# Optimization experiments

Hardware: AMD Instinct MI355X
Metric: run time of the kernel (lower is better)

Reference implementation:

```python
import jax, jax.numpy as jnp
import numpy as np

B, C, S, HEADS, MLP = 8, 128, 32, 8, 512
EPS = 1e-5
SCALE = (C // HEADS) ** -0.5  # dim_head=16 -> 16**-0.5


def setup_inputs() -> dict:
    key = jax.random.key(0)
    ks = jax.random.split(key, 6)
    x = jax.random.normal(ks[0], (B, C, S, S, S), jnp.float32)
    qkv_w = jax.random.normal(ks[1], (3 * C, C), jnp.float32) * 0.02   # Conv3d 1x1x1, no bias
    proj_w = jax.random.normal(ks[2], (C, C), jnp.float32) * 0.02
    proj_b = jnp.zeros((C,), jnp.float32)
    ln1_w = jnp.ones((C, S, S, S), jnp.float32)
    ln1_b = jnp.zeros((C, S, S, S), jnp.float32)
    ln2_w = jnp.ones((C, S, S, S), jnp.float32)
    ln2_b = jnp.zeros((C, S, S, S), jnp.float32)
    mlp_w1 = jax.random.normal(ks[3], (MLP, C), jnp.float32) * 0.02
    mlp_b1 = jnp.zeros((MLP,), jnp.float32)
    mlp_w2 = jax.random.normal(ks[4], (C, MLP), jnp.float32) * 0.02
    mlp_b2 = jnp.zeros((C,), jnp.float32)
    return dict(x=x, qkv_w=qkv_w, proj_w=proj_w, proj_b=proj_b,
                ln1_w=ln1_w, ln1_b=ln1_b, ln2_w=ln2_w, ln2_b=ln2_b,
                mlp_w1=mlp_w1, mlp_b1=mlp_b1, mlp_w2=mlp_w2, mlp_b2=mlp_b2)


def _layernorm_full(x, w, b):
    # LayerNorm over (channel, D, H, W) per batch element, biased variance, eps=1e-5
    mu = jnp.mean(x, axis=(1, 2, 3, 4), keepdims=True)
    var = jnp.mean(jnp.square(x - mu), axis=(1, 2, 3, 4), keepdims=True)
    return (x - mu) * jax.lax.rsqrt(var + EPS) * w[None] + b[None]


def _block(x, qkv_w, proj_w, proj_b, ln1_w, ln1_b, ln2_w, ln2_b,
           mlp_w1, mlp_b1, mlp_w2, mlp_b2):
    b, c, d, h, w = x.shape
    n = d * h * w
    ch = c // HEADS
    xf = x.reshape(b, c, n)
    # 1x1x1 conv == per-voxel matmul over channels
    qkv = jnp.einsum('bcn,oc->bon', xf, qkv_w)                 # [b, 3c, n]
    q, k, v = jnp.split(qkv, 3, axis=1)
    q = q.reshape(b, HEADS, ch, n)
    k = k.reshape(b, HEADS, ch, n)
    v = v.reshape(b, HEADS, ch, n)
    # channel-channel attention: contraction over spatial tokens n
    attn = jax.nn.softmax(jnp.einsum('bhin,bhjn->bhij', q, k) * SCALE, axis=-1)
    out = jnp.einsum('bhij,bhjn->bhin', attn, v).reshape(b, c, n)
    out = jnp.einsum('bcn,oc->bon', out, proj_w) + proj_b[None, :, None]
    x1 = _layernorm_full(x + out.reshape(b, c, d, h, w), ln1_w, ln1_b)
    # MLP: conv1x1 -> exact GELU -> conv1x1
    x1f = x1.reshape(b, c, n)
    hid = jax.nn.gelu(jnp.einsum('bcn,oc->bon', x1f, mlp_w1) + mlp_b1[None, :, None],
                      approximate=False)
    m = jnp.einsum('bon,co->bcn', hid, mlp_w2) + mlp_b2[None, :, None]
    return _layernorm_full(x1 + m.reshape(b, c, d, h, w), ln2_w, ln2_b)


def reference(x, qkv_w, proj_w, proj_b, ln1_w, ln1_b, ln2_w, ln2_b,
              mlp_w1, mlp_b1, mlp_w2, mlp_b2):
    return _block(x, qkv_w, proj_w, proj_b, ln1_w, ln1_b, ln2_w, ln2_b,
                  mlp_w1, mlp_b1, mlp_w2, mlp_b2)
```

## Files before the change

kernel.cpp:

```cpp
#include <hip/hip_runtime.h>
#include <hip/hip_bf16.h>
#include <math.h>


#define N_SP 32768
typedef __hip_bfloat16 bf16;
static const size_t DS = (size_t)128 * N_SP;

typedef __attribute__((ext_vector_type(8))) short s8b;
typedef __attribute__((ext_vector_type(4))) float f4;

__device__ __forceinline__ ushort f2b(float f) {
    __hip_bfloat16 h = __float2bfloat16(f);
    return *reinterpret_cast<ushort*>(&h);
}
__device__ __forceinline__ float b2f(ushort u) {
    unsigned v = ((unsigned)u) << 16;
    float f;
    __builtin_memcpy(&f, &v, 4);
    return f;
}
__device__ __forceinline__ float gelu_f(float h) {
    float u = 1.5957691216057308f * h * fmaf(0.044715f, h * h, 1.0f);
    float e = __expf(u);
    return h * (1.0f - __builtin_amdgcn_rcpf(e + 1.0f));
}
__device__ __forceinline__ int swz8(int n, int c0) {
    return n * 128 + (c0 ^ ((n & 15) << 3));
}
__device__ __forceinline__ int swz4(int n, int c0) {
    return n * 128 + (((c0 & 0x78) ^ ((n & 15) << 3)) | (c0 & 4));
}

__global__ __launch_bounds__(256) void k_transpose(const float* __restrict__ in,
                                                   float* __restrict__ out,
                                                   int R, int Ccols) {
    int idx = blockIdx.x * 256 + threadIdx.x;
    if (idx >= R * Ccols) return;
    int r = idx / Ccols, c = idx % Ccols;
    out[c * R + r] = in[idx];
}

__global__ __launch_bounds__(256) void k_cvt(const float* __restrict__ in,
                                             ushort* __restrict__ out, int n) {
    int i = blockIdx.x * 256 + threadIdx.x;
    if (i < n) out[i] = f2b(in[i]);
}

__global__ __launch_bounds__(256) void k_packln(const float* __restrict__ w,
                                                const float* __restrict__ b,
                                                uint* __restrict__ out) {
    int tid = blockIdx.x * 256 + threadIdx.x;
    int c = tid >> 15, n = tid & 32767;
    uint lo = f2b(w[tid]);
    uint hi = f2b(b[tid]);
    out[(size_t)n * 128 + c] = lo | (hi << 16);
}

__global__ __launch_bounds__(256) void k_packflat(const float* __restrict__ w,
                                                  const float* __restrict__ b,
                                                  uint* __restrict__ out) {
    int tid = blockIdx.x * 256 + threadIdx.x;
    uint lo = f2b(w[tid]);
    uint hi = f2b(b[tid]);
    out[tid] = lo | (hi << 16);
}

__global__ __launch_bounds__(256, 4) void k_cov(const float* __restrict__ x,
                                                float* __restrict__ Gpart) {
    __shared__ ushort xs[128 * 136];
    const int kb = blockIdx.x, b = blockIdx.y;
    const int t = threadIdx.x;
    const int wave = t >> 6, lane = t & 63, q = lane >> 4, r = lane & 15;
    f4 acc[8][2];
#pragma unroll
    for (int m = 0; m < 8; ++m) { acc[m][0] = (f4){0,0,0,0}; acc[m][1] = (f4){0,0,0,0}; }
    for (int ch = 0; ch < 2; ++ch) {
        const int nbase = kb * 256 + ch * 128;
        __syncthreads();
        {
            const int nq = t & 31, cr = t >> 5;
            const float* xp = x + (size_t)b * DS + nbase + nq * 4;
#pragma unroll
            for (int half = 0; half < 2; ++half) {
                float4 xv[8];
#pragma unroll
                for (int cc = 0; cc < 8; ++cc)
                    xv[cc] = *(const float4*)(xp + (size_t)(cr * 16 + half * 8 + cc) * N_SP);
#pragma unroll
                for (int cc = 0; cc < 8; ++cc) {
                    int c = cr * 16 + half * 8 + cc;
                    ushort4 pk;
                    pk.x = f2b(xv[cc].x); pk.y = f2b(xv[cc].y);
                    pk.z = f2b(xv[cc].z); pk.w = f2b(xv[cc].w);
                    *(ushort4*)&xs[c * 136 + nq * 4] = pk;
                }
            }
        }
        __syncthreads();
        for (int kk = 0; kk < 4; ++kk) {
            const int c0 = kk * 32 + q * 8;
            s8b bj0 = *(const s8b*)&xs[(wave * 32 + r) * 136 + c0];
            s8b bj1 = *(const s8b*)&xs[(wave * 32 + 16 + r) * 136 + c0];
#pragma unroll
            for (int m = 0; m < 8; ++m) {
                s8b a = *(const s8b*)&xs[(m * 16 + r) * 136 + c0];
                acc[m][0] = __builtin_amdgcn_mfma_f32_16x16x32_bf16(a, bj0, acc[m][0], 0, 0, 0);
                acc[m][1] = __builtin_amdgcn_mfma_f32_16x16x32_bf16(a, bj1, acc[m][1], 0, 0, 0);
            }
        }
    }
    float* gp = Gpart + ((size_t)b * 128 + kb) * 16384;
#pragma unroll
    for (int n2 = 0; n2 < 2; ++n2)
#pragma unroll
        for (int m = 0; m < 8; ++m)
#pragma unroll
            for (int rg = 0; rg < 4; ++rg) {
                int i = m * 16 + q * 4 + rg;
                int j = wave * 32 + n2 * 16 + r;
                gp[i * 128 + j] = acc[m][n2][rg];
            }
}

__global__ __launch_bounds__(256) void k_greduce(const float* __restrict__ Gpart,
                                                 float* __restrict__ G) {
    int tid = blockIdx.x * 256 + threadIdx.x;
    int b = tid >> 14, ij = tid & 16383;
    float s = 0.f;
#pragma unroll 8
    for (int kb = 0; kb < 128; ++kb)
        s += Gpart[((size_t)b * 128 + kb) * 16384 + ij];
    G[tid] = s;
}

__global__ __launch_bounds__(256) void k_gram_small(const float* __restrict__ G,
                                                    const float* __restrict__ qkv_w,
                                                    float* __restrict__ attn) {
    __shared__ float t1[16 * 132];
    __shared__ float sg[16 * 16];
    const int bh = blockIdx.x;
    const int b = bh >> 3, h = bh & 7;
    const int t = threadIdx.x;
    {
        const int i = t >> 4, c20 = (t & 15) * 8;
        const float* wq = qkv_w + (size_t)(h * 16 + i) * 128;
        const float* Gb = G + (size_t)b * 16384;
        float a[8];
#pragma unroll
        for (int k = 0; k < 8; ++k) a[k] = 0.f;
        for (int c = 0; c < 128; ++c) {
            float w = wq[c];
            const float* grow = Gb + c * 128 + c20;
#pragma unroll
            for (int k = 0; k < 8; ++k) a[k] = fmaf(w, grow[k], a[k]);
        }
#pragma unroll
        for (int k = 0; k < 8; ++k) t1[i * 132 + c20 + k] = a[k];
    }
    __syncthreads();
    {
        const int i = t >> 4, j = t & 15;
        const float* wk = qkv_w + (size_t)(128 + h * 16 + j) * 128;
        float s = 0.f;
        for (int c2 = 0; c2 < 128; ++c2) s = fmaf(t1[i * 132 + c2], wk[c2], s);
        sg[i * 16 + j] = s * 0.25f;
    }
    __syncthreads();
    if (t < 16) {
        float mx = -1e30f;
#pragma unroll
        for (int j = 0; j < 16; ++j) mx = fmaxf(mx, sg[t * 16 + j]);
        float e[16], sum = 0.f;
#pragma unroll
        for (int j = 0; j < 16; ++j) { e[j] = expf(sg[t * 16 + j] - mx); sum += e[j]; }
        float inv = 1.0f / sum;
#pragma unroll
        for (int j = 0; j < 16; ++j)
            attn[((size_t)bh * 16 + t) * 16 + j] = e[j] * inv;
    }
}

__global__ __launch_bounds__(256, 2) void k_mfold(const float* __restrict__ attn,
                                                  const float* __restrict__ qkv_w,
                                                  const float* __restrict__ PT,
                                                  ushort* __restrict__ Mbb) {
    __shared__ float t2[128 * 128];
    const int b = blockIdx.x, t = threadIdx.x;
    {
        const int hi = t >> 1, c0 = (t & 1) * 64;
        const int h = hi >> 4;
        const float* at = attn + ((size_t)b * 128 + hi) * 16;
        float a[16];
#pragma unroll
        for (int j = 0; j < 16; ++j) a[j] = at[j];
        float sc[64];
#pragma unroll
        for (int c = 0; c < 64; ++c) sc[c] = 0.f;
        for (int j = 0; j < 16; ++j) {
            const float* wv = qkv_w + (size_t)(256 + h * 16 + j) * 128 + c0;
            float aj = a[j];
#pragma unroll
            for (int c = 0; c < 64; ++c) sc[c] = fmaf(aj, wv[c], sc[c]);
        }
#pragma unroll
        for (int c = 0; c < 64; ++c) t2[hi * 128 + c0 + c] = sc[c];
    }
    __syncthreads();
    const int c = t & 127, half = t >> 7;
    float acc[128];
#pragma unroll
    for (int o = 0; o < 128; ++o) acc[o] = 0.f;
    for (int ci = half * 64; ci < half * 64 + 64; ++ci) {
        float s = t2[ci * 128 + c];
        const float* pt = PT + ci * 128;
#pragma unroll
        for (int o = 0; o < 128; ++o) acc[o] = fmaf(pt[o], s, acc[o]);
    }
    __syncthreads();
    if (half) {
#pragma unroll
        for (int o = 0; o < 128; ++o) t2[c * 128 + o] = acc[o];
    }
    __syncthreads();
    if (!half) {
        ushort* m = Mbb + (size_t)b * 16384;
#pragma unroll
        for (int o = 0; o < 128; ++o)
            m[(size_t)o * 128 + c] = f2b(acc[o] + t2[c * 128 + o]);
    }
}

__global__ __launch_bounds__(256, 3) void k_attnproj(const float* __restrict__ x,
                                                     const ushort* __restrict__ Mbb,
                                                     const float* __restrict__ proj_b,
                                                     ushort* __restrict__ x1Tb,
                                                     float* __restrict__ st) {
    __shared__ ushort xT[128 * 136];
    const int b = blockIdx.y;
    const int n0 = blockIdx.x * 128;
    const int t = threadIdx.x;
    const int wave = t >> 6, lane = t & 63, q = lane >> 4, r = lane & 15;
    {
        const int nn = t & 127, cg = t >> 7;
        const float* xp = x + (size_t)b * DS + n0 + nn;
        for (int gb = 0; gb < 4; ++gb) {
            float xv[16];
#pragma unroll
            for (int u = 0; u < 16; ++u)
                xv[u] = xp[(size_t)(cg * 64 + gb * 16 + u) * N_SP];
#pragma unroll
            for (int u4 = 0; u4 < 4; ++u4) {
                int c0 = cg * 64 + gb * 16 + u4 * 4;
                ushort4 pk;
                pk.x = f2b(xv[u4 * 4 + 0]); pk.y = f2b(xv[u4 * 4 + 1]);
                pk.z = f2b(xv[u4 * 4 + 2]); pk.w = f2b(xv[u4 * 4 + 3]);
                *(ushort4*)&xT[nn * 136 + c0] = pk;
            }
        }
    }
    const int orow = wave * 32 + r;
    s8b a[8];
    {
        const ushort* mp = Mbb + (size_t)b * 16384 + (size_t)orow * 128 + q * 8;
#pragma unroll
        for (int m = 0; m < 2; ++m)
#pragma unroll
            for (int kk = 0; kk < 4; ++kk)
                a[m * 4 + kk] = *(const s8b*)(mp + m * 16 * 128 + kk * 32);
    }
    __syncthreads();
    f4 acc[2][8];
#pragma unroll
    for (int m = 0; m < 2; ++m)
#pragma unroll
        for (int j = 0; j < 8; ++j) acc[m][j] = (f4){0,0,0,0};
#pragma unroll
    for (int kk = 0; kk < 4; ++kk) {
        const int c0 = kk * 32 + q * 8;
#pragma unroll
        for (int j = 0; j < 8; ++j) {
            s8b bx = *(const s8b*)&xT[(j * 16 + r) * 136 + c0];
            acc[0][j] = __builtin_amdgcn_mfma_f32_16x16x32_bf16(a[kk],     bx, acc[0][j], 0, 0, 0);
            acc[1][j] = __builtin_amdgcn_mfma_f32_16x16x32_bf16(a[4 + kk], bx, acc[1][j], 0, 0, 0);
        }
    }
    float s = 0.f, sq = 0.f;
    float4 pbq0 = *(const float4*)&proj_b[wave * 32 + q * 4];
    float4 pbq1 = *(const float4*)&proj_b[wave * 32 + 16 + q * 4];
#pragma unroll
    for (int m = 0; m < 2; ++m) {
        const int o0 = wave * 32 + m * 16 + q * 4;
        const float4 pb = m ? pbq1 : pbq0;
#pragma unroll
        for (int j = 0; j < 8; ++j) {
            const int nn = j * 16 + r;
            ushort4 xr = *(const ushort4*)&xT[nn * 136 + o0];
            float v0 = acc[m][j][0] + pb.x + b2f(xr.x);
            float v1 = acc[m][j][1] + pb.y + b2f(xr.y);
            float v2 = acc[m][j][2] + pb.z + b2f(xr.z);
            float v3 = acc[m][j][3] + pb.w + b2f(xr.w);
            ushort4 ov;
            ov.x = f2b(v0); ov.y = f2b(v1); ov.z = f2b(v2); ov.w = f2b(v3);
            *(ushort4*)(x1Tb + (size_t)b * DS + (size_t)(n0 + nn) * 128 + o0) = ov;
            s += (v0 + v1) + (v2 + v3);
            sq = fmaf(v0, v0, sq); sq = fmaf(v1, v1, sq);
            sq = fmaf(v2, v2, sq); sq = fmaf(v3, v3, sq);
        }
    }
#pragma unroll
    for (int off = 32; off > 0; off >>= 1) {
        s += __shfl_down(s, off, 64);
        sq += __shfl_down(sq, off, 64);
    }
    if (lane == 0) {
        atomicAdd(&st[0 + b], s);
        atomicAdd(&st[8 + b], sq);
    }
}

__global__ void k_finalize(float* st, int off) {
    int b = threadIdx.x;
    if (b < 8) {
        const float invn = 1.0f / 4194304.0f;
        float mu = st[off + b] * invn;
        float var = st[off + 8 + b] * invn - mu * mu;
        st[off + 16 + b] = mu;
        st[off + 24 + b] = rsqrtf(var + 1e-5f);
    }
}

__global__ __launch_bounds__(256) void k_lnapply(const float* __restrict__ in,
                                                 const uint* __restrict__ lnwb,
                                                 const float* __restrict__ st, int off,
                                                 float* __restrict__ out) {
    size_t i4 = (size_t)blockIdx.x * 256 + threadIdx.x;
    int b = (int)(i4 >> 20);
    size_t cn = i4 * 4 - (size_t)b * 4194304;
    float mu = st[off + 16 + b], rs = st[off + 24 + b];
    const float4 xv = *(const float4*)(in + (size_t)b * DS + cn);
    const uint4 wv = *(const uint4*)(lnwb + cn);
    float4 o;
    o.x = fmaf((xv.x - mu) * rs, b2f((ushort)(wv.x & 0xffffu)), b2f((ushort)(wv.x >> 16)));
    o.y = fmaf((xv.y - mu) * rs, b2f((ushort)(wv.y & 0xffffu)), b2f((ushort)(wv.y >> 16)));
    o.z = fmaf((xv.z - mu) * rs, b2f((ushort)(wv.z & 0xffffu)), b2f((ushort)(wv.z >> 16)));
    o.w = fmaf((xv.w - mu) * rs, b2f((ushort)(wv.w & 0xffffu)), b2f((ushort)(wv.w >> 16)));
    *(float4*)(out + (size_t)b * DS + cn) = o;
}

__global__ __launch_bounds__(256, 2) void k_mlp(const ushort* __restrict__ x1Tb,
                                                float* __restrict__ xout,
                                                const ushort* __restrict__ w1b,
                                                const float* __restrict__ b1v,
                                                const ushort* __restrict__ w2b,
                                                const float* __restrict__ b2v,
                                                const uint* __restrict__ lnwbT,
                                                float* __restrict__ st) {
    __shared__ ushort xT[128 * 128];
    __shared__ ushort hT[128 * 128];
    const int b = blockIdx.y;
    const int n0 = blockIdx.x * 128;
    const int t = threadIdx.x;
    const int wave = t >> 6, lane = t & 63, q = lane >> 4, r = lane & 15;
    const float mu = st[16 + b], rs = st[24 + b];
    {
        const int c8 = (t & 15) * 8, rb = t >> 4;
        const ushort* xb = x1Tb + (size_t)b * DS + (size_t)n0 * 128;
        const uint*  wb = lnwbT + (size_t)n0 * 128;
#pragma unroll
        for (int gb = 0; gb < 2; ++gb) {
            s8b xv[4]; uint4 wv0[4], wv1[4];
#pragma unroll
            for (int u = 0; u < 4; ++u) {
                int nn = (gb * 4 + u) * 16 + rb;
                xv[u]  = *(const s8b*)(xb + (size_t)nn * 128 + c8);
                wv0[u] = *(const uint4*)(wb + (size_t)nn * 128 + c8);
                wv1[u] = *(const uint4*)(wb + (size_t)nn * 128 + c8 + 4);
            }
#pragma unroll
            for (int u = 0; u < 4; ++u) {
                int nn = (gb * 4 + u) * 16 + rb;
                ushort4 p0, p1;
                float xe;
                xe = b2f((ushort)xv[u][0]);
                p0.x = f2b(fmaf((xe - mu) * rs, b2f((ushort)(wv0[u].x & 0xffffu)), b2f((ushort)(wv0[u].x >> 16))));
                xe = b2f((ushort)xv[u][1]);
                p0.y = f2b(fmaf((xe - mu) * rs, b2f((ushort)(wv0[u].y & 0xffffu)), b2f((ushort)(wv0[u].y >> 16))));
                xe = b2f((ushort)xv[u][2]);
                p0.z = f2b(fmaf((xe - mu) * rs, b2f((ushort)(wv0[u].z & 0xffffu)), b2f((ushort)(wv0[u].z >> 16))));
                xe = b2f((ushort)xv[u][3]);
                p0.w = f2b(fmaf((xe - mu) * rs, b2f((ushort)(wv0[u].w & 0xffffu)), b2f((ushort)(wv0[u].w >> 16))));
                xe = b2f((ushort)xv[u][4]);
                p1.x = f2b(fmaf((xe - mu) * rs, b2f((ushort)(wv1[u].x & 0xffffu)), b2f((ushort)(wv1[u].x >> 16))));
                xe = b2f((ushort)xv[u][5]);
                p1.y = f2b(fmaf((xe - mu) * rs, b2f((ushort)(wv1[u].y & 0xffffu)), b2f((ushort)(wv1[u].y >> 16))));
                xe = b2f((ushort)xv[u][6]);
                p1.z = f2b(fmaf((xe - mu) * rs, b2f((ushort)(wv1[u].z & 0xffffu)), b2f((ushort)(wv1[u].z >> 16))));
                xe = b2f((ushort)xv[u][7]);
                p1.w = f2b(fmaf((xe - mu) * rs, b2f((ushort)(wv1[u].w & 0xffffu)), b2f((ushort)(wv1[u].w >> 16))));
                *(ushort4*)&xT[swz4(nn, c8)] = p0;
                *(ushort4*)&xT[swz4(nn, c8 + 4)] = p1;
            }
        }
    }
    const int orow = wave * 32 + r;
    s8b a1[8];
    {
        const ushort* w1p = w1b + (size_t)orow * 128 + q * 8;
#pragma unroll
        for (int m = 0; m < 2; ++m)
#pragma unroll
            for (int kk = 0; kk < 4; ++kk)
                a1[m * 4 + kk] = *(const s8b*)(w1p + m * 16 * 128 + kk * 32);
    }
    __syncthreads();
    f4 acc2[2][8];
#pragma unroll
    for (int m = 0; m < 2; ++m)
#pragma unroll
        for (int j = 0; j < 8; ++j) acc2[m][j] = (f4){0,0,0,0};

    for (int os = 0; os < 4; ++os) {
        f4 acc1[2][8];
#pragma unroll
        for (int m = 0; m < 2; ++m)
#pragma unroll
            for (int j = 0; j < 8; ++j) acc1[m][j] = (f4){0,0,0,0};
#pragma unroll
        for (int kk = 0; kk < 4; ++kk) {
            const int c0 = kk * 32 + q * 8;
#pragma unroll
            for (int j = 0; j < 8; ++j) {
                s8b bx = *(const s8b*)&xT[swz8(j * 16 + r, c0)];
                acc1[0][j] = __builtin_amdgcn_mfma_f32_16x16x32_bf16(a1[kk],     bx, acc1[0][j], 0, 0, 0);
                acc1[1][j] = __builtin_amdgcn_mfma_f32_16x16x32_bf16(a1[4 + kk], bx, acc1[1][j], 0, 0, 0);
            }
        }
        s8b a2[8];
        {
            const ushort* w2p = w2b + (size_t)orow * 512 + os * 128 + q * 8;
#pragma unroll
            for (int m = 0; m < 2; ++m)
#pragma unroll
                for (int kk = 0; kk < 4; ++kk)
                    a2[m * 4 + kk] = *(const s8b*)(w2p + m * 16 * 512 + kk * 32);
        }
        float4 b1q0 = *(const float4*)&b1v[os * 128 + wave * 32 + q * 4];
        float4 b1q1 = *(const float4*)&b1v[os * 128 + wave * 32 + 16 + q * 4];
#pragma unroll
        for (int m = 0; m < 2; ++m) {
            const int hr0 = wave * 32 + m * 16 + q * 4;
            const float4 bq = m ? b1q1 : b1q0;
#pragma unroll
            for (int j = 0; j < 8; ++j) {
                ushort4 pk;
                pk.x = f2b(gelu_f(acc1[m][j][0] + bq.x));
                pk.y = f2b(gelu_f(acc1[m][j][1] + bq.y));
                pk.z = f2b(gelu_f(acc1[m][j][2] + bq.z));
                pk.w = f2b(gelu_f(acc1[m][j][3] + bq.w));
                *(ushort4*)&hT[swz4(j * 16 + r, hr0)] = pk;
            }
        }
        __syncthreads();
#pragma unroll
        for (int kk = 0; kk < 4; ++kk) {
            const int c0 = kk * 32 + q * 8;
#pragma unroll
            for (int j = 0; j < 8; ++j) {
                s8b hx = *(const s8b*)&hT[swz8(j * 16 + r, c0)];
                acc2[0][j] = __builtin_amdgcn_mfma_f32_16x16x32_bf16(a2[kk],     hx, acc2[0][j], 0, 0, 0);
                acc2[1][j] = __builtin_amdgcn_mfma_f32_16x16x32_bf16(a2[4 + kk], hx, acc2[1][j], 0, 0, 0);
            }
        }
        if (os < 3) {
            const ushort* w1p = w1b + (size_t)((os + 1) * 128 + orow) * 128 + q * 8;
#pragma unroll
            for (int m = 0; m < 2; ++m)
#pragma unroll
                for (int kk = 0; kk < 4; ++kk)
                    a1[m * 4 + kk] = *(const s8b*)(w1p + m * 16 * 128 + kk * 32);
        }
        __syncthreads();
    }
    float s = 0.f, sq = 0.f;
    float4 b2q0 = *(const float4*)&b2v[wave * 32 + q * 4];
    float4 b2q1 = *(const float4*)&b2v[wave * 32 + 16 + q * 4];
#pragma unroll
    for (int m = 0; m < 2; ++m) {
        const int o0 = wave * 32 + m * 16 + q * 4;
        const float4 bq = m ? b2q1 : b2q0;
#pragma unroll
        for (int j = 0; j < 8; ++j) {
            const int nn = j * 16 + r;
            ushort4 xr = *(const ushort4*)&xT[swz4(nn, o0)];
            float v0 = acc2[m][j][0] + bq.x + b2f(xr.x);
            float v1 = acc2[m][j][1] + bq.y + b2f(xr.y);
            float v2 = acc2[m][j][2] + bq.z + b2f(xr.z);
            float v3 = acc2[m][j][3] + bq.w + b2f(xr.w);
            float* op = xout + (size_t)b * DS + n0 + nn;
            op[(size_t)(o0 + 0) * N_SP] = v0;
            op[(size_t)(o0 + 1) * N_SP] = v1;
            op[(size_t)(o0 + 2) * N_SP] = v2;
            op[(size_t)(o0 + 3) * N_SP] = v3;
            s += (v0 + v1) + (v2 + v3);
            sq = fmaf(v0, v0, sq); sq = fmaf(v1, v1, sq);
            sq = fmaf(v2, v2, sq); sq = fmaf(v3, v3, sq);
        }
    }
#pragma unroll
    for (int off = 32; off > 0; off >>= 1) {
        s += __shfl_down(s, off, 64);
        sq += __shfl_down(sq, off, 64);
    }
    if (lane == 0) {
        atomicAdd(&st[32 + b], s);
        atomicAdd(&st[40 + b], sq);
    }
}

extern "C" void kernel_launch(void* const* d_in, const int* in_sizes, int n_in,
                              void* d_out, int out_size, void* d_ws, size_t ws_size,
                              hipStream_t stream) {
    const float* x      = (const float*)d_in[0];
    const float* qkv_w  = (const float*)d_in[1];
    const float* proj_w = (const float*)d_in[2];
    const float* proj_b = (const float*)d_in[3];
    const float* ln1_w  = (const float*)d_in[4];
    const float* ln1_b  = (const float*)d_in[5];
    const float* ln2_w  = (const float*)d_in[6];
    const float* ln2_b  = (const float*)d_in[7];
    const float* mlp_w1 = (const float*)d_in[8];
    const float* mlp_b1 = (const float*)d_in[9];
    const float* mlp_w2 = (const float*)d_in[10];
    const float* mlp_b2 = (const float*)d_in[11];
    float* out = (float*)d_out;

    char* wsb = (char*)d_ws;
    float*  st    = (float*)wsb;
    float*  attn  = (float*)(wsb + 256);
    float*  PT    = (float*)(wsb + 65792);
    ushort* Mbb   = (ushort*)(wsb + 131328);
    ushort* w1b   = (ushort*)(wsb + 393472);
    ushort* w2b   = (ushort*)(wsb + 524544);
    float*  G     = (float*)(wsb + 655616);
    uint*   lnwbT = (uint*)(wsb + 1179904);
    float*  Gpart = (float*)(wsb + 18874368);
    ushort* x1Tb  = (ushort*)(wsb + 18874368);
    uint*   lnwb2 = (uint*)(wsb + 18874368);

    hipMemsetAsync(st, 0, 64 * sizeof(float), stream);

    k_transpose<<<64, 256, 0, stream>>>(proj_w, PT, 128, 128);
    k_cvt<<<256, 256, 0, stream>>>(mlp_w1, w1b, 65536);
    k_cvt<<<256, 256, 0, stream>>>(mlp_w2, w2b, 65536);
    k_packln<<<16384, 256, 0, stream>>>(ln1_w, ln1_b, lnwbT);

    k_cov<<<dim3(128, 8), 256, 0, stream>>>(x, Gpart);
    k_greduce<<<512, 256, 0, stream>>>(Gpart, G);
    k_gram_small<<<64, 256, 0, stream>>>(G, qkv_w, attn);
    k_mfold<<<8, 256, 0, stream>>>(attn, qkv_w, PT, Mbb);

    k_attnproj<<<dim3(256, 8), 256, 0, stream>>>(x, Mbb, proj_b, x1Tb, st);
    k_finalize<<<1, 64, 0, stream>>>(st, 0);
    k_mlp<<<dim3(256, 8), 256, 0, stream>>>(x1Tb, out, w1b, mlp_b1, w2b, mlp_b2,
                                            lnwbT, st);
    k_packflat<<<16384, 256, 0, stream>>>(ln2_w, ln2_b, lnwb2);
    k_finalize<<<1, 64, 0, stream>>>(st, 32);
    k_lnapply<<<32768, 256, 0, stream>>>(out, lnwb2, st, 32, out);
}
```

Before: 970.6 us.

## Halve cov partials, vectorize x transpose loads, add nontemporal hints, fold biases into accumulators

k_cov now handles 512 spatial positions per block with a grid of 64 instead of 128, halving the Gpart partial buffer and the reduction work in k_greduce. k_attnproj loads x with float4 reads instead of scalar strided reads and transposes in registers. Many streaming loads and stores (x, x1Tb, LN weights, output) use nontemporal hints to reduce cache pollution. MLP biases are now the initial accumulator values, which removes the per-element bias adds. Trade-offs are less parallelism in k_cov and more register pressure in the vectorized transpose.

Measured after the change: 953.3 us. Within noise of the previous version (-1.8%).

```diff
diff --git a/kernel.cpp b/kernel.cpp
--- a/kernel.cpp
+++ b/kernel.cpp
@@ -9,6 +9,8 @@
 
 typedef __attribute__((ext_vector_type(8))) short s8b;
 typedef __attribute__((ext_vector_type(4))) float f4;
+typedef __attribute__((ext_vector_type(4))) uint u4v;
+typedef __attribute__((ext_vector_type(4))) ushort us4v;
 
 __device__ __forceinline__ ushort f2b(float f) {
     __hip_bfloat16 h = __float2bfloat16(f);
@@ -75,18 +77,19 @@
     f4 acc[8][2];
 #pragma unroll
     for (int m = 0; m < 8; ++m) { acc[m][0] = (f4){0,0,0,0}; acc[m][1] = (f4){0,0,0,0}; }
-    for (int ch = 0; ch < 2; ++ch) {
-        const int nbase = kb * 256 + ch * 128;
+    for (int ch = 0; ch < 4; ++ch) {
+        const int nbase = kb * 512 + ch * 128;
         __syncthreads();
         {
             const int nq = t & 31, cr = t >> 5;
             const float* xp = x + (size_t)b * DS + nbase + nq * 4;
 #pragma unroll
             for (int half = 0; half < 2; ++half) {
-                float4 xv[8];
+                f4 xv[8];
 #pragma unroll
                 for (int cc = 0; cc < 8; ++cc)
-                    xv[cc] = *(const float4*)(xp + (size_t)(cr * 16 + half * 8 + cc) * N_SP);
+                    xv[cc] = __builtin_nontemporal_load(
+                        (const f4*)(xp + (size_t)(cr * 16 + half * 8 + cc) * N_SP));
 #pragma unroll
                 for (int cc = 0; cc < 8; ++cc) {
                     int c = cr * 16 + half * 8 + cc;
@@ -110,7 +113,7 @@
             }
         }
     }
-    float* gp = Gpart + ((size_t)b * 128 + kb) * 16384;
+    float* gp = Gpart + ((size_t)b * 64 + kb) * 16384;
 #pragma unroll
     for (int n2 = 0; n2 < 2; ++n2)
 #pragma unroll
@@ -129,8 +132,8 @@
     int b = tid >> 14, ij = tid & 16383;
     float s = 0.f;
 #pragma unroll 8
-    for (int kb = 0; kb < 128; ++kb)
-        s += Gpart[((size_t)b * 128 + kb) * 16384 + ij];
+    for (int kb = 0; kb < 64; ++kb)
+        s += __builtin_nontemporal_load(&Gpart[((size_t)b * 64 + kb) * 16384 + ij]);
     G[tid] = s;
 }
 
@@ -242,20 +245,26 @@
     const int t = threadIdx.x;
     const int wave = t >> 6, lane = t & 63, q = lane >> 4, r = lane & 15;
     {
-        const int nn = t & 127, cg = t >> 7;
-        const float* xp = x + (size_t)b * DS + n0 + nn;
-        for (int gb = 0; gb < 4; ++gb) {
-            float xv[16];
-#pragma unroll
-            for (int u = 0; u < 16; ++u)
-                xv[u] = xp[(size_t)(cg * 64 + gb * 16 + u) * N_SP];
-#pragma unroll
-            for (int u4 = 0; u4 < 4; ++u4) {
-                int c0 = cg * 64 + gb * 16 + u4 * 4;
-                ushort4 pk;
-                pk.x = f2b(xv[u4 * 4 + 0]); pk.y = f2b(xv[u4 * 4 + 1]);
-                pk.z = f2b(xv[u4 * 4 + 2]); pk.w = f2b(xv[u4 * 4 + 3]);
-                *(ushort4*)&xT[nn * 136 + c0] = pk;
+        const int nq = (t & 31) * 4;
+        const int cg = (t >> 5) * 4;
+        const float* xb = x + (size_t)b * DS + n0 + nq;
+#pragma unroll
+        for (int ph = 0; ph < 2; ++ph) {
+            f4 xv[8];
+#pragma unroll
+            for (int u = 0; u < 8; ++u) {
+                int c = ph * 64 + cg + (u >> 2) * 32 + (u & 3);
+                xv[u] = __builtin_nontemporal_load((const f4*)(xb + (size_t)c * N_SP));
+            }
+#pragma unroll
+            for (int u2 = 0; u2 < 2; ++u2) {
+                int c0 = ph * 64 + cg + u2 * 32;
+#pragma unroll
+                for (int i = 0; i < 4; ++i) {
+                    us4v pk = { f2b(xv[u2 * 4 + 0][i]), f2b(xv[u2 * 4 + 1][i]),
+                                f2b(xv[u2 * 4 + 2][i]), f2b(xv[u2 * 4 + 3][i]) };
+                    *(us4v*)&xT[(nq + i) * 136 + c0] = pk;
+                }
             }
         }
     }
@@ -300,9 +309,9 @@
             float v1 = acc[m][j][1] + pb.y + b2f(xr.y);
             float v2 = acc[m][j][2] + pb.z + b2f(xr.z);
             float v3 = acc[m][j][3] + pb.w + b2f(xr.w);
-            ushort4 ov;
-            ov.x = f2b(v0); ov.y = f2b(v1); ov.z = f2b(v2); ov.w = f2b(v3);
-            *(ushort4*)(x1Tb + (size_t)b * DS + (size_t)(n0 + nn) * 128 + o0) = ov;
+            us4v ov = { f2b(v0), f2b(v1), f2b(v2), f2b(v3) };
+            __builtin_nontemporal_store(ov,
+                (us4v*)(x1Tb + (size_t)b * DS + (size_t)(n0 + nn) * 128 + o0));
             s += (v0 + v1) + (v2 + v3);
             sq = fmaf(v0, v0, sq); sq = fmaf(v1, v1, sq);
             sq = fmaf(v2, v2, sq); sq = fmaf(v3, v3, sq);
@@ -369,13 +378,13 @@
         const uint*  wb = lnwbT + (size_t)n0 * 128;
 #pragma unroll
         for (int gb = 0; gb < 2; ++gb) {
-            s8b xv[4]; uint4 wv0[4], wv1[4];
+            s8b xv[4]; u4v wv0[4], wv1[4];
 #pragma unroll
             for (int u = 0; u < 4; ++u) {
                 int nn = (gb * 4 + u) * 16 + rb;
-                xv[u]  = *(const s8b*)(xb + (size_t)nn * 128 + c8);
-                wv0[u] = *(const uint4*)(wb + (size_t)nn * 128 + c8);
-                wv1[u] = *(const uint4*)(wb + (size_t)nn * 128 + c8 + 4);
+                xv[u]  = __builtin_nontemporal_load((const s8b*)(xb + (size_t)nn * 128 + c8));
+                wv0[u] = __builtin_nontemporal_load((const u4v*)(wb + (size_t)nn * 128 + c8));
+                wv1[u] = __builtin_nontemporal_load((const u4v*)(wb + (size_t)nn * 128 + c8 + 4));
             }
 #pragma unroll
             for (int u = 0; u < 4; ++u) {
@@ -414,18 +423,24 @@
                 a1[m * 4 + kk] = *(const s8b*)(w1p + m * 16 * 128 + kk * 32);
     }
     __syncthreads();
+    float4 b2q0 = *(const float4*)&b2v[wave * 32 + q * 4];
+    float4 b2q1 = *(const float4*)&b2v[wave * 32 + 16 + q * 4];
     f4 acc2[2][8];
 #pragma unroll
-    for (int m = 0; m < 2; ++m)
-#pragma unroll
-        for (int j = 0; j < 8; ++j) acc2[m][j] = (f4){0,0,0,0};
+    for (int j = 0; j < 8; ++j) {
+        acc2[0][j] = (f4){b2q0.x, b2q0.y, b2q0.z, b2q0.w};
+        acc2[1][j] = (f4){b2q1.x, b2q1.y, b2q1.z, b2q1.w};
+    }
 
     for (int os = 0; os < 4; ++os) {
+        float4 b1q0 = *(const float4*)&b1v[os * 128 + wave * 32 + q * 4];
+        float4 b1q1 = *(const float4*)&b1v[os * 128 + wave * 32 + 16 + q * 4];
         f4 acc1[2][8];
 #pragma unroll
-        for (int m = 0; m < 2; ++m)
-#pragma unroll
-            for (int j = 0; j < 8; ++j) acc1[m][j] = (f4){0,0,0,0};
+        for (int j = 0; j < 8; ++j) {
+            acc1[0][j] = (f4){b1q0.x, b1q0.y, b1q0.z, b1q0.w};
+            acc1[1][j] = (f4){b1q1.x, b1q1.y, b1q1.z, b1q1.w};
+        }
 #pragma unroll
         for (int kk = 0; kk < 4; ++kk) {
             const int c0 = kk * 32 + q * 8;
@@ -445,19 +460,16 @@
                 for (int kk = 0; kk < 4; ++kk)
                     a2[m * 4 + kk] = *(const s8b*)(w2p + m * 16 * 512 + kk * 32);
         }
-        float4 b1q0 = *(const float4*)&b1v[os * 128 + wave * 32 + q * 4];
-        float4 b1q1 = *(const float4*)&b1v[os * 128 + wave * 32 + 16 + q * 4];
 #pragma unroll
         for (int m = 0; m < 2; ++m) {
             const int hr0 = wave * 32 + m * 16 + q * 4;
-            const float4 bq = m ? b1q1 : b1q0;
 #pragma unroll
             for (int j = 0; j < 8; ++j) {
                 ushort4 pk;
-                pk.x = f2b(gelu_f(acc1[m][j][0] + bq.x));
-                pk.y = f2b(gelu_f(acc1[m][j][1] + bq.y));
-                pk.z = f2b(gelu_f(acc1[m][j][2] + bq.z));
-                pk.w = f2b(gelu_f(acc1[m][j][3] + bq.w));
+                pk.x = f2b(gelu_f(acc1[m][j][0]));
+                pk.y = f2b(gelu_f(acc1[m][j][1]));
+                pk.z = f2b(gelu_f(acc1[m][j][2]));
+                pk.w = f2b(gelu_f(acc1[m][j][3]));
                 *(ushort4*)&hT[swz4(j * 16 + r, hr0)] = pk;
             }
         }
@@ -483,25 +495,22 @@
         __syncthreads();
     }
     float s = 0.f, sq = 0.f;
-    float4 b2q0 = *(const float4*)&b2v[wave * 32 + q * 4];
-    float4 b2q1 = *(const float4*)&b2v[wave * 32 + 16 + q * 4];
 #pragma unroll
     for (int m = 0; m < 2; ++m) {
         const int o0 = wave * 32 + m * 16 + q * 4;
-        const float4 bq = m ? b2q1 : b2q0;
 #pragma unroll
         for (int j = 0; j < 8; ++j) {
             const int nn = j * 16 + r;
             ushort4 xr = *(const ushort4*)&xT[swz4(nn, o0)];
-            float v0 = acc2[m][j][0] + bq.x + b2f(xr.x);
-            float v1 = acc2[m][j][1] + bq.y + b2f(xr.y);
-            float v2 = acc2[m][j][2] + bq.z + b2f(xr.z);
-            float v3 = acc2[m][j][3] + bq.w + b2f(xr.w);
+            float v0 = acc2[m][j][0] + b2f(xr.x);
+            float v1 = acc2[m][j][1] + b2f(xr.y);
+            float v2 = acc2[m][j][2] + b2f(xr.z);
+            float v3 = acc2[m][j][3] + b2f(xr.w);
             float* op = xout + (size_t)b * DS + n0 + nn;
-            op[(size_t)(o0 + 0) * N_SP] = v0;
-            op[(size_t)(o0 + 1) * N_SP] = v1;
-            op[(size_t)(o0 + 2) * N_SP] = v2;
-            op[(size_t)(o0 + 3) * N_SP] = v3;
+            __builtin_nontemporal_store(v0, op + (size_t)(o0 + 0) * N_SP);
+            __builtin_nontemporal_store(v1, op + (size_t)(o0 + 1) * N_SP);
+            __builtin_nontemporal_store(v2, op + (size_t)(o0 + 2) * N_SP);
+            __builtin_nontemporal_store(v3, op + (size_t)(o0 + 3) * N_SP);
             s += (v0 + v1) + (v2 + v3);
             sq = fmaf(v0, v0, sq); sq = fmaf(v1, v1, sq);
             sq = fmaf(v2, v2, sq); sq = fmaf(v3, v3, sq);
@@ -555,7 +564,7 @@
     k_cvt<<<256, 256, 0, stream>>>(mlp_w2, w2b, 65536);
     k_packln<<<16384, 256, 0, stream>>>(ln1_w, ln1_b, lnwbT);
 
-    k_cov<<<dim3(128, 8), 256, 0, stream>>>(x, Gpart);
+    k_cov<<<dim3(64, 8), 256, 0, stream>>>(x, Gpart);
     k_greduce<<<512, 256, 0, stream>>>(Gpart, G);
     k_gram_small<<<64, 256, 0, stream>>>(G, qkv_w, attn);
     k_mfold<<<8, 256, 0, stream>>>(attn, qkv_w, PT, Mbb);
```
